# Optimization experiments

Hardware: AMD Instinct MI355X
Metric: run time of the kernel (lower is better)

Reference implementation:

```python
import jax, jax.numpy as jnp
import numpy as np

M1, M2, M3 = 16, 16, 3  # Fourier mode truncation (modes3 hard-coded to 3 in torch __init__)


def setup_inputs() -> dict:
    key = jax.random.key(0)
    k0, k1, k2, k3, k4 = jax.random.split(key, 5)
    B, Ci, Co, T, X, P = 8, 32, 32, 128, 256, 3
    scale = 1.0 / (Ci * Co)
    x = jax.random.normal(k0, (B, Ci, T, X, P), dtype=jnp.float32)
    w1_re = scale * jax.random.uniform(k1, (Ci, Co, M1, M2, M3), dtype=jnp.float32)
    w1_im = scale * jax.random.uniform(k2, (Ci, Co, M1, M2, M3), dtype=jnp.float32)
    w2_re = scale * jax.random.uniform(k3, (Ci, Co, M1, M2, M3), dtype=jnp.float32)
    w2_im = scale * jax.random.uniform(k4, (Ci, Co, M1, M2, M3), dtype=jnp.float32)
    return {"x": x, "w1_re": w1_re, "w1_im": w1_im, "w2_re": w2_re, "w2_im": w2_im}


def reference(x, w1_re, w1_im, w2_re, w2_im):
    # x: [B, Ci, T, X, P] -- pipes pre-stacked along last dim (method == 34 branch)
    B, Ci, T, X, P = x.shape
    Co = w1_re.shape[1]
    w1 = (w1_re + 1j * w1_im).astype(jnp.complex64)
    w2 = (w2_re + 1j * w2_im).astype(jnp.complex64)

    x_ft = jnp.fft.rfftn(x, axes=(2, 3, 4))          # [B, Ci, T, X, P//2+1]
    z = min(x_ft.shape[4], M3)                       # torch: z_dim = min(x_ft.shape[4], modes3)

    # low-x / low-y corner
    coeff1 = jnp.zeros((B, Ci, M1, M2, M3), jnp.complex64)
    coeff1 = coeff1.at[..., :z].set(x_ft[:, :, :M1, :M2, :z])
    blk1 = jnp.einsum('bixyz,ioxyz->boxyz', coeff1, w1)

    # high-x / low-y corner
    coeff2 = jnp.zeros((B, Ci, M1, M2, M3), jnp.complex64)
    coeff2 = coeff2.at[..., :z].set(x_ft[:, :, -M1:, :M2, :z])
    blk2 = jnp.einsum('bixyz,ioxyz->boxyz', coeff2, w2)

    out_ft = jnp.zeros((B, Co, T, X, P), jnp.complex64)
    out_ft = out_ft.at[:, :, :M1, :M2, :M3].set(blk1)
    out_ft = out_ft.at[:, :, -M1:, :M2, :M3].set(blk2)

    # irfftn with s=(T, X, P) crops last axis to P//2+1 coeffs, matching torch semantics
    out = jnp.fft.irfftn(out_ft, s=(T, X, P), axes=(-3, -2, -1))  # [B, Co, T, X, P] float32
    return out
```

## Files before the change

kernel.cpp:

```cpp
#include <hip/hip_runtime.h>
#include <math.h>

typedef float2 F2;

__device__ __forceinline__ F2 cmul(F2 a, F2 b) {
    return make_float2(a.x * b.x - a.y * b.y, a.x * b.y + a.y * b.x);
}
__device__ __forceinline__ F2 cmac(F2 acc, F2 a, F2 b) {
    acc.x += a.x * b.x - a.y * b.y;
    acc.y += a.x * b.y + a.y * b.x;
    return acc;
}

#define TWO_PI 6.283185307179586f
#define SQRT3_2 0.8660254037844386f
#define SQRT3 1.7320508075688772f

__global__ __launch_bounds__(256) void k1_fwd_x(const float* __restrict__ x,
                                                F2* __restrict__ y) {
    __shared__ float xp0[8][257];
    __shared__ F2    xp1[8][257];
    __shared__ F2    tw[256];
    __shared__ F2    part[1024];
    const int tid = threadIdx.x;
    const int blk = blockIdx.x;

    {
        float sv, cv;
        sincosf(-TWO_PI * (float)tid * (1.0f / 256.0f), &sv, &cv);
        tw[tid] = make_float2(cv, sv);
    }
#pragma unroll
    for (int j = 0; j < 8; ++j) {
        int item = tid + 256 * j;
        int row = item >> 8, xx = item & 255;
        const float* src = x + ((size_t)(blk * 8 + row) * 256 + xx) * 3;
        float a = src[0], b = src[1], c = src[2];
        xp0[row][xx] = a + b + c;
        xp1[row][xx] = make_float2(a - 0.5f * (b + c), SQRT3_2 * (c - b));
    }
    __syncthreads();

    const int kz = tid >> 7, rr = (tid >> 4) & 7, kxg = (tid >> 2) & 3, c = tid & 3;
    const float sgn = (kxg & 1) ? -1.0f : 1.0f;

    F2 acc[4], w[4], stp[4];
#pragma unroll
    for (int u = 0; u < 4; ++u) {
        int kx = kxg + 4 * u;
        acc[u] = make_float2(0.f, 0.f);
        w[u] = tw[(kx * c) & 255];
        stp[u] = tw[(4 * kx) & 255];
    }

    if (kz == 0) {
        const float* r0 = xp0[rr];
#pragma unroll 8
        for (int m = 0; m < 32; ++m) {
            int xx = c + 4 * m;
            float s = fmaf(sgn, r0[xx + 128], r0[xx]);
#pragma unroll
            for (int u = 0; u < 4; ++u) {
                acc[u].x = fmaf(s, w[u].x, acc[u].x);
                acc[u].y = fmaf(s, w[u].y, acc[u].y);
                w[u] = cmul(w[u], stp[u]);
            }
        }
    } else {
        const F2* r1 = xp1[rr];
#pragma unroll 8
        for (int m = 0; m < 32; ++m) {
            int xx = c + 4 * m;
            F2 a = r1[xx], b = r1[xx + 128];
            F2 s = make_float2(fmaf(sgn, b.x, a.x), fmaf(sgn, b.y, a.y));
#pragma unroll
            for (int u = 0; u < 4; ++u) {
                acc[u] = cmac(acc[u], s, w[u]);
                w[u] = cmul(w[u], stp[u]);
            }
        }
    }

#pragma unroll
    for (int u = 0; u < 4; ++u) {
        int kx = kxg + 4 * u;
        part[(((rr * 2 + kz) * 16 + kx) << 2) + c] = acc[u];
    }
    __syncthreads();
    {
        int rr2 = tid >> 5, kz2 = (tid >> 4) & 1, kx2 = tid & 15;
        const F2* p = &part[((rr2 * 2 + kz2) * 16 + kx2) << 2];
        F2 r = p[0];
        r.x += p[1].x + p[2].x + p[3].x;
        r.y += p[1].y + p[2].y + p[3].y;
        y[((size_t)(blk * 8 + rr2) * 2 + kz2) * 16 + kx2] = r;
    }
}

__global__ __launch_bounds__(256) void k2a_fwd_t(const F2* __restrict__ y,
                                                 F2* __restrict__ xft) {
    __shared__ F2 yL[128][16];
    const int tid = threadIdx.x;
    const int bi = blockIdx.x >> 1, kz = blockIdx.x & 1;
#pragma unroll
    for (int j = 0; j < 8; ++j) {
        int item = tid + 256 * j;
        int t = item >> 4, kx = item & 15;
        yL[t][kx] = y[((size_t)(bi * 128 + t) * 2 + kz) * 16 + kx];
    }
    __syncthreads();

    const int kx = tid & 15, sg = tid >> 4;
    F2 rotA = make_float2(1.f, 0.f), rotB = make_float2(1.f, 0.f), stepA, stepB;
    sincosf(-TWO_PI * (float)sg * (1.0f / 128.0f), &stepA.y, &stepA.x);
    sincosf(-TWO_PI * (float)(112 + sg) * (1.0f / 128.0f), &stepB.y, &stepB.x);
    F2 accA = make_float2(0.f, 0.f), accB = make_float2(0.f, 0.f);
    for (int t = 0; t < 128; ++t) {
        F2 v = yL[t][kx];
        accA = cmac(accA, v, rotA);
        accB = cmac(accB, v, rotB);
        rotA = cmul(rotA, stepA);
        rotB = cmul(rotB, stepB);
    }
    const int b = bi >> 5, i = bi & 31;
    xft[(((size_t)(b * 32 + sg) * 2 + kz) * 16 + kx) * 32 + i] = accA;
    xft[(((size_t)(b * 32 + (16 + sg)) * 2 + kz) * 16 + kx) * 32 + i] = accB;
}

__global__ __launch_bounds__(256) void k2b_mix(const F2* __restrict__ xft,
                                               const float* __restrict__ w1re,
                                               const float* __restrict__ w1im,
                                               const float* __restrict__ w2re,
                                               const float* __restrict__ w2im,
                                               F2* __restrict__ blkout) {
    __shared__ F2 xL[512];
    __shared__ F2 wcL[2][32][32];
    const int tid = threadIdx.x;
    const int s = blockIdx.x >> 4, kx = blockIdx.x & 15;
#pragma unroll
    for (int j = 0; j < 2; ++j) {
        int item = tid + 256 * j;
        int b = item >> 6, kz = (item >> 5) & 1, i = item & 31;
        xL[item] = xft[(((size_t)(b * 32 + s) * 2 + kz) * 16 + kx) * 32 + i];
    }
    const float* bre = (s < 16) ? w1re : w2re;
    const float* bim = (s < 16) ? w1im : w2im;
    const int m1 = s & 15;
#pragma unroll
    for (int j = 0; j < 4; ++j) {
        int iop = tid + 256 * j;
        int i = iop >> 5, o = iop & 31;
        size_t g = (((size_t)(i * 32 + o) * 16 + m1) * 16 + kx) * 3;
        wcL[0][i][o] = make_float2(bre[g], bim[g]);
        wcL[1][i][o] = make_float2(bre[g + 1], bim[g + 1]);
    }
    __syncthreads();

    const int b = tid >> 5, o = tid & 31;
#pragma unroll
    for (int kz = 0; kz < 2; ++kz) {
        F2 acc = make_float2(0.f, 0.f);
        for (int i = 0; i < 32; ++i) {
            F2 xv = xL[(b * 2 + kz) * 32 + i];
            F2 wv = wcL[kz][i][o];
            acc.x += xv.x * wv.x - xv.y * wv.y;
            acc.y += xv.x * wv.y + xv.y * wv.x;
        }
        blkout[(((size_t)(b * 32 + o) * 32 + s) * 2 + kz) * 16 + kx] = acc;
    }
}

__global__ __launch_bounds__(256) void k2c_inv_t(const F2* __restrict__ blkin,
                                                 F2* __restrict__ h) {
    __shared__ F2 bL[1024];
    const int tid = threadIdx.x;
    const int bo = blockIdx.x >> 2, tc = blockIdx.x & 3;
#pragma unroll
    for (int j = 0; j < 4; ++j) {
        int item = tid + 256 * j;
        bL[item] = blkin[(size_t)bo * 1024 + item];
    }
    __syncthreads();

    const int col = tid & 31, tl = tid >> 5;
    F2 accA[4], accB[4], w[4], stp[4];
#pragma unroll
    for (int q = 0; q < 4; ++q) {
        accA[q] = make_float2(0.f, 0.f);
        accB[q] = make_float2(0.f, 0.f);
        w[q] = make_float2(1.f, 0.f);
        int t = 32 * tc + tl + 8 * q;
        sincosf(TWO_PI * (float)t * (1.0f / 128.0f), &stp[q].y, &stp[q].x);
    }
    for (int sp = 0; sp < 16; ++sp) {
        F2 bA = bL[sp * 32 + col];
        F2 bB = bL[(16 + sp) * 32 + col];
#pragma unroll
        for (int q = 0; q < 4; ++q) {
            accA[q] = cmac(accA[q], bA, w[q]);
            accB[q] = cmac(accB[q], bB, w[q]);
            w[q] = cmul(w[q], stp[q]);
        }
    }
    F2 phase;
    sincosf(-TWO_PI * (float)tl * (1.0f / 8.0f), &phase.y, &phase.x);
#pragma unroll
    for (int q = 0; q < 4; ++q) {
        int t = 32 * tc + tl + 8 * q;
        F2 r = cmac(accA[q], phase, accB[q]);
        h[((size_t)bo * 128 + t) * 32 + col] = r;
    }
}

__global__ __launch_bounds__(256) void k3_inv_x(const F2* __restrict__ h,
                                                float* __restrict__ out) {
    __shared__ F2 hL[64];
    const int tid = threadIdx.x;
    const int blk = blockIdx.x;
    if (tid < 64) hL[tid] = h[(size_t)blk * 64 + tid];
    __syncthreads();

    const int rr = tid >> 7, x = tid & 127;
    const F2* hrow = &hL[rr * 32];
    F2 w = make_float2(1.f, 0.f), r;
    sincosf(TWO_PI * (float)x * (1.0f / 256.0f), &r.y, &r.x);
    float e0 = 0.f, o0 = 0.f;
    F2 e1 = make_float2(0.f, 0.f), o1 = make_float2(0.f, 0.f);
#pragma unroll
    for (int k2 = 0; k2 < 8; ++k2) {
        {
            F2 h0 = hrow[2 * k2], h1 = hrow[16 + 2 * k2];
            e0 += h0.x * w.x - h0.y * w.y;
            e1.x += h1.x * w.x - h1.y * w.y;
            e1.y += h1.x * w.y + h1.y * w.x;
            w = cmul(w, r);
        }
        {
            F2 h0 = hrow[2 * k2 + 1], h1 = hrow[16 + 2 * k2 + 1];
            o0 += h0.x * w.x - h0.y * w.y;
            o1.x += h1.x * w.x - h1.y * w.y;
            o1.y += h1.x * w.y + h1.y * w.x;
            w = cmul(w, r);
        }
    }
    const float n = 1.0f / 98304.0f;
    float* dst = out + ((size_t)blk * 2 + rr) * 768;
    {
        float g0 = e0 + o0, g1r = e1.x + o1.x, g1i = e1.y + o1.y;
        dst[x * 3 + 0] = n * (g0 + 2.f * g1r);
        dst[x * 3 + 1] = n * (g0 - g1r - SQRT3 * g1i);
        dst[x * 3 + 2] = n * (g0 - g1r + SQRT3 * g1i);
    }
    {
        float g0 = e0 - o0, g1r = e1.x - o1.x, g1i = e1.y - o1.y;
        int xb = x + 128;
        dst[xb * 3 + 0] = n * (g0 + 2.f * g1r);
        dst[xb * 3 + 1] = n * (g0 - g1r - SQRT3 * g1i);
        dst[xb * 3 + 2] = n * (g0 - g1r + SQRT3 * g1i);
    }
}

extern "C" void kernel_launch(void* const* d_in, const int* in_sizes, int n_in,
                              void* d_out, int out_size, void* d_ws, size_t ws_size,
                              hipStream_t stream) {
    const float* x    = (const float*)d_in[0];
    const float* w1re = (const float*)d_in[1];
    const float* w1im = (const float*)d_in[2];
    const float* w2re = (const float*)d_in[3];
    const float* w2im = (const float*)d_in[4];
    float* out = (float*)d_out;

    F2* y   = (F2*)d_ws;
    F2* xft = y + 1048576;
    F2* bk  = xft + 262144;
    F2* h   = bk + 262144;

    hipLaunchKernelGGL(k1_fwd_x,  dim3(4096),  dim3(256), 0, stream, x, y);
    hipLaunchKernelGGL(k2a_fwd_t, dim3(512),   dim3(256), 0, stream, y, xft);
    hipLaunchKernelGGL(k2b_mix,   dim3(512),   dim3(256), 0, stream, xft,
                       w1re, w1im, w2re, w2im, bk);
    hipLaunchKernelGGL(k2c_inv_t, dim3(1024),  dim3(256), 0, stream, bk, h);
    hipLaunchKernelGGL(k3_inv_x,  dim3(16384), dim3(256), 0, stream, h, out);
}
```

Baseline: 264.0 us.

## Fuse inverse T/X stages, repack weights, and use shuffle reduction in forward X

Merges the inverse-T and inverse-X kernels into one so the intermediate h stays in shared memory, and stages output through LDS for coalesced float4 stores. Adds a weight-packing kernel that reorders weights into contiguous complex pairs, so the mix kernel loads them with coalesced reads. The forward-X kernel now uses 8 lanes per row with wavefront shuffles instead of a shared-memory partial reduction, and pads its shared rows. The extra packing kernel runs on every call and adds weight traffic, and the larger register footprint may reduce occupancy.

```diff
diff --git a/kernel.cpp b/kernel.cpp
--- a/kernel.cpp
+++ b/kernel.cpp
@@ -16,19 +16,46 @@
 #define SQRT3_2 0.8660254037844386f
 #define SQRT3 1.7320508075688772f
 
-__global__ __launch_bounds__(256) void k1_fwd_x(const float* __restrict__ x,
-                                                F2* __restrict__ y) {
-    __shared__ float xp0[8][257];
-    __shared__ F2    xp1[8][257];
-    __shared__ F2    tw[256];
-    __shared__ F2    part[1024];
+__global__ __launch_bounds__(256) void kw_pack(const float* __restrict__ w1re,
+                                               const float* __restrict__ w1im,
+                                               const float* __restrict__ w2re,
+                                               const float* __restrict__ w2im,
+                                               F2* __restrict__ p1,
+                                               F2* __restrict__ p2) {
+    const int tid = threadIdx.x;
+    const int blk = blockIdx.x;
+    const bool second = blk >= 768;
+    const float* re = second ? w2re : w1re;
+    const float* im = second ? w2im : w1im;
+    F2* dstp = second ? p2 : p1;
+    const int base = (second ? blk - 768 : blk) * 1024;
+#pragma unroll
+    for (int j = 0; j < 4; ++j) {
+        int e = base + tid + 256 * j;
+        float rv = re[e], iv = im[e];
+        int m3 = e % 3;
+        int r = e / 3;
+        int kx = r & 15;
+        int m1 = (r >> 4) & 15;
+        int io = r >> 8;
+        if (m3 < 2) {
+            dstp[(size_t)(((m1 * 16 + kx) * 2 + m3) * 1024 + io)] = make_float2(rv, iv);
+        }
+    }
+}
+
+__global__ __launch_bounds__(256, 5) void k1_fwd_x(const float* __restrict__ x,
+                                                   F2* __restrict__ y) {
+    __shared__ float xp0[8][264];
+    __shared__ F2    xp1[8][264];
+    __shared__ F2    twred[256];
     const int tid = threadIdx.x;
     const int blk = blockIdx.x;
 
     {
         float sv, cv;
         sincosf(-TWO_PI * (float)tid * (1.0f / 256.0f), &sv, &cv);
-        tw[tid] = make_float2(cv, sv);
+        twred[tid] = make_float2(cv, sv);
     }
 #pragma unroll
     for (int j = 0; j < 8; ++j) {
@@ -41,26 +68,26 @@
     }
     __syncthreads();
 
-    const int kz = tid >> 7, rr = (tid >> 4) & 7, kxg = (tid >> 2) & 3, c = tid & 3;
-    const float sgn = (kxg & 1) ? -1.0f : 1.0f;
-
-    F2 acc[4], w[4], stp[4];
-#pragma unroll
-    for (int u = 0; u < 4; ++u) {
-        int kx = kxg + 4 * u;
+    const int c8 = tid & 7, kxg = (tid >> 3) & 1, rr = (tid >> 4) & 7, kz = tid >> 7;
+    const float sgn = kxg ? -1.0f : 1.0f;
+
+    F2 acc[8], w[8], stp[8];
+#pragma unroll
+    for (int u = 0; u < 8; ++u) {
+        int kx = kxg + 2 * u;
         acc[u] = make_float2(0.f, 0.f);
-        w[u] = tw[(kx * c) & 255];
-        stp[u] = tw[(4 * kx) & 255];
+        w[u] = twred[(kx * c8) & 255];
+        stp[u] = twred[(8 * kx) & 255];
     }
 
     if (kz == 0) {
         const float* r0 = xp0[rr];
-#pragma unroll 8
-        for (int m = 0; m < 32; ++m) {
-            int xx = c + 4 * m;
+#pragma unroll 4
+        for (int m = 0; m < 16; ++m) {
+            int xx = c8 + 8 * m;
             float s = fmaf(sgn, r0[xx + 128], r0[xx]);
 #pragma unroll
-            for (int u = 0; u < 4; ++u) {
+            for (int u = 0; u < 8; ++u) {
                 acc[u].x = fmaf(s, w[u].x, acc[u].x);
                 acc[u].y = fmaf(s, w[u].y, acc[u].y);
                 w[u] = cmul(w[u], stp[u]);
@@ -68,13 +95,13 @@
         }
     } else {
         const F2* r1 = xp1[rr];
-#pragma unroll 8
-        for (int m = 0; m < 32; ++m) {
-            int xx = c + 4 * m;
+#pragma unroll 4
+        for (int m = 0; m < 16; ++m) {
+            int xx = c8 + 8 * m;
             F2 a = r1[xx], b = r1[xx + 128];
             F2 s = make_float2(fmaf(sgn, b.x, a.x), fmaf(sgn, b.y, a.y));
 #pragma unroll
-            for (int u = 0; u < 4; ++u) {
+            for (int u = 0; u < 8; ++u) {
                 acc[u] = cmac(acc[u], s, w[u]);
                 w[u] = cmul(w[u], stp[u]);
             }
@@ -82,19 +109,21 @@
     }
 
 #pragma unroll
-    for (int u = 0; u < 4; ++u) {
-        int kx = kxg + 4 * u;
-        part[(((rr * 2 + kz) * 16 + kx) << 2) + c] = acc[u];
-    }
-    __syncthreads();
-    {
-        int rr2 = tid >> 5, kz2 = (tid >> 4) & 1, kx2 = tid & 15;
-        const F2* p = &part[((rr2 * 2 + kz2) * 16 + kx2) << 2];
-        F2 r = p[0];
-        r.x += p[1].x + p[2].x + p[3].x;
-        r.y += p[1].y + p[2].y + p[3].y;
-        y[((size_t)(blk * 8 + rr2) * 2 + kz2) * 16 + kx2] = r;
-    }
+    for (int u = 0; u < 8; ++u) {
+#pragma unroll
+        for (int d = 1; d <= 4; d <<= 1) {
+            acc[u].x += __shfl_xor(acc[u].x, d, 64);
+            acc[u].y += __shfl_xor(acc[u].y, d, 64);
+        }
+    }
+    __syncthreads();
+    if (c8 == 0) {
+#pragma unroll
+        for (int u = 0; u < 8; ++u)
+            twred[((rr * 2 + kz) << 4) + kxg + 2 * u] = acc[u];
+    }
+    __syncthreads();
+    y[(size_t)blk * 256 + tid] = twred[tid];
 }
 
 __global__ __launch_bounds__(256) void k2a_fwd_t(const F2* __restrict__ y,
@@ -128,13 +157,11 @@
 }
 
 __global__ __launch_bounds__(256) void k2b_mix(const F2* __restrict__ xft,
-                                               const float* __restrict__ w1re,
-                                               const float* __restrict__ w1im,
-                                               const float* __restrict__ w2re,
-                                               const float* __restrict__ w2im,
+                                               const F2* __restrict__ p1,
+                                               const F2* __restrict__ p2,
                                                F2* __restrict__ blkout) {
     __shared__ F2 xL[512];
-    __shared__ F2 wcL[2][32][32];
+    __shared__ F2 wcL[2][1024];
     const int tid = threadIdx.x;
     const int s = blockIdx.x >> 4, kx = blockIdx.x & 15;
 #pragma unroll
@@ -143,16 +170,13 @@
         int b = item >> 6, kz = (item >> 5) & 1, i = item & 31;
         xL[item] = xft[(((size_t)(b * 32 + s) * 2 + kz) * 16 + kx) * 32 + i];
     }
-    const float* bre = (s < 16) ? w1re : w2re;
-    const float* bim = (s < 16) ? w1im : w2im;
+    const F2* wsrc = (s < 16) ? p1 : p2;
     const int m1 = s & 15;
-#pragma unroll
-    for (int j = 0; j < 4; ++j) {
-        int iop = tid + 256 * j;
-        int i = iop >> 5, o = iop & 31;
-        size_t g = (((size_t)(i * 32 + o) * 16 + m1) * 16 + kx) * 3;
-        wcL[0][i][o] = make_float2(bre[g], bim[g]);
-        wcL[1][i][o] = make_float2(bre[g + 1], bim[g + 1]);
+    const size_t wbase = (size_t)(m1 * 16 + kx) * 2048;
+#pragma unroll
+    for (int j = 0; j < 8; ++j) {
+        int item = tid + 256 * j;
+        wcL[0][item] = wsrc[wbase + item];
     }
     __syncthreads();
 
@@ -162,7 +186,7 @@
         F2 acc = make_float2(0.f, 0.f);
         for (int i = 0; i < 32; ++i) {
             F2 xv = xL[(b * 2 + kz) * 32 + i];
-            F2 wv = wcL[kz][i][o];
+            F2 wv = wcL[kz][i * 32 + o];
             acc.x += xv.x * wv.x - xv.y * wv.y;
             acc.y += xv.x * wv.y + xv.y * wv.x;
         }
@@ -170,93 +194,103 @@
     }
 }
 
-__global__ __launch_bounds__(256) void k2c_inv_t(const F2* __restrict__ blkin,
-                                                 F2* __restrict__ h) {
+__global__ __launch_bounds__(256, 4) void k2c3(const F2* __restrict__ bkin,
+                                               float* __restrict__ out) {
     __shared__ F2 bL[1024];
-    const int tid = threadIdx.x;
-    const int bo = blockIdx.x >> 2, tc = blockIdx.x & 3;
+    __shared__ F2 hL[16][33];
+    __shared__ float oL[2][772];
+    const int tid = threadIdx.x;
+    const int bo = blockIdx.x >> 3, tc = blockIdx.x & 7;
 #pragma unroll
     for (int j = 0; j < 4; ++j) {
         int item = tid + 256 * j;
-        bL[item] = blkin[(size_t)bo * 1024 + item];
-    }
-    __syncthreads();
-
-    const int col = tid & 31, tl = tid >> 5;
-    F2 accA[4], accB[4], w[4], stp[4];
-#pragma unroll
-    for (int q = 0; q < 4; ++q) {
-        accA[q] = make_float2(0.f, 0.f);
-        accB[q] = make_float2(0.f, 0.f);
-        w[q] = make_float2(1.f, 0.f);
-        int t = 32 * tc + tl + 8 * q;
-        sincosf(TWO_PI * (float)t * (1.0f / 128.0f), &stp[q].y, &stp[q].x);
-    }
-    for (int sp = 0; sp < 16; ++sp) {
-        F2 bA = bL[sp * 32 + col];
-        F2 bB = bL[(16 + sp) * 32 + col];
-#pragma unroll
-        for (int q = 0; q < 4; ++q) {
-            accA[q] = cmac(accA[q], bA, w[q]);
-            accB[q] = cmac(accB[q], bB, w[q]);
-            w[q] = cmul(w[q], stp[q]);
-        }
-    }
-    F2 phase;
-    sincosf(-TWO_PI * (float)tl * (1.0f / 8.0f), &phase.y, &phase.x);
-#pragma unroll
-    for (int q = 0; q < 4; ++q) {
-        int t = 32 * tc + tl + 8 * q;
-        F2 r = cmac(accA[q], phase, accB[q]);
-        h[((size_t)bo * 128 + t) * 32 + col] = r;
-    }
-}
-
-__global__ __launch_bounds__(256) void k3_inv_x(const F2* __restrict__ h,
-                                                float* __restrict__ out) {
-    __shared__ F2 hL[64];
-    const int tid = threadIdx.x;
-    const int blk = blockIdx.x;
-    if (tid < 64) hL[tid] = h[(size_t)blk * 64 + tid];
-    __syncthreads();
-
-    const int rr = tid >> 7, x = tid & 127;
-    const F2* hrow = &hL[rr * 32];
-    F2 w = make_float2(1.f, 0.f), r;
-    sincosf(TWO_PI * (float)x * (1.0f / 256.0f), &r.y, &r.x);
-    float e0 = 0.f, o0 = 0.f;
-    F2 e1 = make_float2(0.f, 0.f), o1 = make_float2(0.f, 0.f);
-#pragma unroll
-    for (int k2 = 0; k2 < 8; ++k2) {
+        bL[item] = bkin[(size_t)bo * 1024 + item];
+    }
+    __syncthreads();
+
+    {
+        const int col = tid & 31, tl = tid >> 5;
+        F2 accA[2], accB[2], w[2], stp[2];
+#pragma unroll
+        for (int q = 0; q < 2; ++q) {
+            accA[q] = make_float2(0.f, 0.f);
+            accB[q] = make_float2(0.f, 0.f);
+            w[q] = make_float2(1.f, 0.f);
+            int t = tc * 16 + tl + 8 * q;
+            sincosf(TWO_PI * (float)t * (1.0f / 128.0f), &stp[q].y, &stp[q].x);
+        }
+        for (int sp = 0; sp < 16; ++sp) {
+            F2 bA = bL[sp * 32 + col];
+            F2 bB = bL[(16 + sp) * 32 + col];
+#pragma unroll
+            for (int q = 0; q < 2; ++q) {
+                accA[q] = cmac(accA[q], bA, w[q]);
+                accB[q] = cmac(accB[q], bB, w[q]);
+                w[q] = cmul(w[q], stp[q]);
+            }
+        }
+        F2 ph;
+        sincosf(-TWO_PI * (float)tl * (1.0f / 8.0f), &ph.y, &ph.x);
+#pragma unroll
+        for (int q = 0; q < 2; ++q) {
+            F2 r = cmac(accA[q], ph, accB[q]);
+            hL[tl + 8 * q][col] = r;
+        }
+    }
+    __syncthreads();
+
+    const int xx = tid & 127, half = tid >> 7;
+    F2 rot;
+    sincosf(TWO_PI * (float)xx * (1.0f / 256.0f), &rot.y, &rot.x);
+    const float n = 1.0f / 98304.0f;
+    const size_t outbase = (size_t)(bo * 128 + tc * 16) * 768;
+
+    for (int tt = 0; tt < 8; ++tt) {
+        const int t_loc = 2 * tt + half;
+        const F2* hrow = hL[t_loc];
+        F2 w = make_float2(1.f, 0.f);
+        float e0 = 0.f, o0 = 0.f;
+        F2 e1 = make_float2(0.f, 0.f), o1 = make_float2(0.f, 0.f);
+#pragma unroll
+        for (int k2 = 0; k2 < 8; ++k2) {
+            {
+                F2 h0 = hrow[2 * k2], h1 = hrow[16 + 2 * k2];
+                e0 += h0.x * w.x - h0.y * w.y;
+                e1.x += h1.x * w.x - h1.y * w.y;
+                e1.y += h1.x * w.y + h1.y * w.x;
+                w = cmul(w, rot);
+            }
+            {
+                F2 h0 = hrow[2 * k2 + 1], h1 = hrow[16 + 2 * k2 + 1];
+                o0 += h0.x * w.x - h0.y * w.y;
+                o1.x += h1.x * w.x - h1.y * w.y;
+                o1.y += h1.x * w.y + h1.y * w.x;
+                w = cmul(w, rot);
+            }
+        }
+        float* dst = oL[half];
         {
-            F2 h0 = hrow[2 * k2], h1 = hrow[16 + 2 * k2];
-            e0 += h0.x * w.x - h0.y * w.y;
-            e1.x += h1.x * w.x - h1.y * w.y;
-            e1.y += h1.x * w.y + h1.y * w.x;
-            w = cmul(w, r);
+            float g0 = e0 + o0, g1r = e1.x + o1.x, g1i = e1.y + o1.y;
+            dst[xx * 3 + 0] = n * (g0 + 2.f * g1r);
+            dst[xx * 3 + 1] = n * (g0 - g1r - SQRT3 * g1i);
+            dst[xx * 3 + 2] = n * (g0 - g1r + SQRT3 * g1i);
         }
         {
-            F2 h0 = hrow[2 * k2 + 1], h1 = hrow[16 + 2 * k2 + 1];
-            o0 += h0.x * w.x - h0.y * w.y;
-            o1.x += h1.x * w.x - h1.y * w.y;
-            o1.y += h1.x * w.y + h1.y * w.x;
-            w = cmul(w, r);
-        }
-    }
-    const float n = 1.0f / 98304.0f;
-    float* dst = out + ((size_t)blk * 2 + rr) * 768;
-    {
-        float g0 = e0 + o0, g1r = e1.x + o1.x, g1i = e1.y + o1.y;
-        dst[x * 3 + 0] = n * (g0 + 2.f * g1r);
-        dst[x * 3 + 1] = n * (g0 - g1r - SQRT3 * g1i);
-        dst[x * 3 + 2] = n * (g0 - g1r + SQRT3 * g1i);
-    }
-    {
-        float g0 = e0 - o0, g1r = e1.x - o1.x, g1i = e1.y - o1.y;
-        int xb = x + 128;
-        dst[xb * 3 + 0] = n * (g0 + 2.f * g1r);
-        dst[xb * 3 + 1] = n * (g0 - g1r - SQRT3 * g1i);
-        dst[xb * 3 + 2] = n * (g0 - g1r + SQRT3 * g1i);
+            float g0 = e0 - o0, g1r = e1.x - o1.x, g1i = e1.y - o1.y;
+            int xb = xx + 128;
+            dst[xb * 3 + 0] = n * (g0 + 2.f * g1r);
+            dst[xb * 3 + 1] = n * (g0 - g1r - SQRT3 * g1i);
+            dst[xb * 3 + 2] = n * (g0 - g1r + SQRT3 * g1i);
+        }
+        __syncthreads();
+        if (tid < 192) {
+#pragma unroll
+            for (int r = 0; r < 2; ++r) {
+                float4 v = *(const float4*)&oL[r][tid * 4];
+                *(float4*)&out[outbase + (size_t)(2 * tt + r) * 768 + tid * 4] = v;
+            }
+        }
+        __syncthreads();
     }
 }
 
@@ -273,12 +307,13 @@
     F2* y   = (F2*)d_ws;
     F2* xft = y + 1048576;
     F2* bk  = xft + 262144;
-    F2* h   = bk + 262144;
-
-    hipLaunchKernelGGL(k1_fwd_x,  dim3(4096),  dim3(256), 0, stream, x, y);
-    hipLaunchKernelGGL(k2a_fwd_t, dim3(512),   dim3(256), 0, stream, y, xft);
-    hipLaunchKernelGGL(k2b_mix,   dim3(512),   dim3(256), 0, stream, xft,
-                       w1re, w1im, w2re, w2im, bk);
-    hipLaunchKernelGGL(k2c_inv_t, dim3(1024),  dim3(256), 0, stream, bk, h);
-    hipLaunchKernelGGL(k3_inv_x,  dim3(16384), dim3(256), 0, stream, h, out);
-}
+    F2* p1  = bk + 262144;
+    F2* p2  = p1 + 524288;
+
+    hipLaunchKernelGGL(kw_pack,   dim3(1536), dim3(256), 0, stream,
+                       w1re, w1im, w2re, w2im, p1, p2);
+    hipLaunchKernelGGL(k1_fwd_x,  dim3(4096), dim3(256), 0, stream, x, y);
+    hipLaunchKernelGGL(k2a_fwd_t, dim3(512),  dim3(256), 0, stream, y, xft);
+    hipLaunchKernelGGL(k2b_mix,   dim3(512),  dim3(256), 0, stream, xft, p1, p2, bk);
+    hipLaunchKernelGGL(k2c3,      dim3(2048), dim3(256), 0, stream, bk, out);
+}
```

Measured after the change: 316.2 us. 19.8% more time.
